# Performance work log

Measured on AMD Instinct MI355X. Metric: run time of the kernel, lower is better.

Reference implementation:

```python
import jax, jax.numpy as jnp
import numpy as np

D = 8  # polynomial degree; with bias present, basis has D columns (P1..PD)


def setup_inputs() -> dict:
    key = jax.random.key(0)
    k1, k2 = jax.random.split(key)
    batch, n_in, n_out = 65536, 256, 64
    x = jax.random.normal(k1, (batch, n_in), dtype=jnp.float32)
    c_basis = jax.random.normal(k2, (n_out, n_in, D), dtype=jnp.float32) * (1.0 / np.sqrt(n_in * D))
    bias = jnp.zeros((n_out,), dtype=jnp.float32)
    return {"x": x, "c_basis": c_basis, "bias": bias}


def _legendre_basis(x):
    # x: (batch, n_in). Returns (batch, n_in, D) = [P1(t), ..., PD(t)], t = tanh(x).
    t = jnp.tanh(x)
    p_prev = jnp.ones_like(t)  # P0
    p_curr = t                 # P1
    polys = [p_curr]
    for k in range(2, D + 1):  # small fixed-length loop over degree
        p_next = ((2 * k - 1) * t * p_curr - (k - 1) * p_prev) / k
        polys.append(p_next)
        p_prev, p_curr = p_curr, p_next
    return jnp.stack(polys, axis=-1)  # (batch, n_in, D)


def reference(x, c_basis, bias):
    # basis: (batch, n_in, D); contract over (n_in, D) with c_basis (n_out, n_in, D)
    leg = _legendre_basis(x)
    y = jnp.einsum('bid,oid->bo', leg, c_basis)
    return y + bias
```

## Files before the change

kernel.cpp:

```cpp
#include <hip/hip_runtime.h>
#include <hip/hip_bf16.h>

typedef _Float16 half2v __attribute__((ext_vector_type(2)));
typedef _Float16 half8  __attribute__((ext_vector_type(8)));
typedef __attribute__((ext_vector_type(4))) float floatx4;
typedef __attribute__((ext_vector_type(4))) unsigned int uintx4;

#define GLOBAL_AS __attribute__((address_space(1)))
#define LDS_AS __attribute__((address_space(3)))

__device__ __forceinline__ void async_ld16(const void* g, void* l) {
  __builtin_amdgcn_global_load_lds((const GLOBAL_AS unsigned int*)g,
                                   (LDS_AS unsigned int*)l, 16, 0, 0);
}

__device__ __forceinline__ half2v h2(float v) {
  return (half2v){(_Float16)v, (_Float16)v};
}

__device__ __forceinline__ void legendre2_f16(float xv0, float xv1,
                                              half8* fa0, half8* fa1) {
  float e0 = __builtin_amdgcn_exp2f(xv0 * 2.885390081777927f);
  float t0 = 1.0f - 2.0f * __builtin_amdgcn_rcpf(e0 + 1.0f);
  float e1 = __builtin_amdgcn_exp2f(xv1 * 2.885390081777927f);
  float t1 = 1.0f - 2.0f * __builtin_amdgcn_rcpf(e1 + 1.0f);
  half2v t;
  { auto tt = __builtin_amdgcn_cvt_pkrtz(t0, t1); __builtin_memcpy(&t, &tt, 4); }
  half2v p1 = t;
  half2v u2 = t * p1, w2 = u2 - h2(1.0f);  half2v p2 = h2(0.5f)      * w2 + u2;
  half2v u3 = t * p2, w3 = u3 - p1;        half2v p3 = h2(2.0f/3.0f) * w3 + u3;
  half2v u4 = t * p3, w4 = u4 - p2;        half2v p4 = h2(0.75f)     * w4 + u4;
  half2v u5 = t * p4, w5 = u5 - p3;        half2v p5 = h2(0.8f)      * w5 + u5;
  half2v u6 = t * p5, w6 = u6 - p4;        half2v p6 = h2(5.0f/6.0f) * w6 + u6;
  half2v u7 = t * p6, w7 = u7 - p5;        half2v p7 = h2(6.0f/7.0f) * w7 + u7;
  half2v u8 = t * p7, w8 = u8 - p6;        half2v p8 = h2(7.0f/8.0f) * w8 + u8;
  unsigned P[8];
  __builtin_memcpy(&P[0], &p1, 4); __builtin_memcpy(&P[1], &p2, 4);
  __builtin_memcpy(&P[2], &p3, 4); __builtin_memcpy(&P[3], &p4, 4);
  __builtin_memcpy(&P[4], &p5, 4); __builtin_memcpy(&P[5], &p6, 4);
  __builtin_memcpy(&P[6], &p7, 4); __builtin_memcpy(&P[7], &p8, 4);
  union { unsigned u[4]; half8 h; } a0, a1;
#pragma unroll
  for (int j = 0; j < 4; ++j) {
    a0.u[j] = __builtin_amdgcn_perm(P[2*j+1], P[2*j], 0x05040100u);
    a1.u[j] = __builtin_amdgcn_perm(P[2*j+1], P[2*j], 0x07060302u);
  }
  *fa0 = a0.h;
  *fa1 = a1.h;
}

__global__ void conv_kernel(const float* __restrict__ cb, _Float16* __restrict__ ws) {
  int t = blockIdx.x * 128 + threadIdx.x;
  int o = t >> 8;
  int i = t & 255;
  const floatx4* s = (const floatx4*)(cb + ((size_t)o * 256 + i) * 8);
  floatx4 v0 = s[0], v1 = s[1];
  union { _Float16 h[8]; uintx4 u; } w;
  w.h[0] = (_Float16)v0.x; w.h[1] = (_Float16)v0.y;
  w.h[2] = (_Float16)v0.z; w.h[3] = (_Float16)v0.w;
  w.h[4] = (_Float16)v1.x; w.h[5] = (_Float16)v1.y;
  w.h[6] = (_Float16)v1.z; w.h[7] = (_Float16)v1.w;
  *(uintx4*)(ws + (size_t)i * 512 + o * 8) = w.u;
}

#define MB 64
#define NCH 16

__global__ __launch_bounds__(128, 2) void kan_kernel(
    const float* __restrict__ x, const _Float16* __restrict__ ws,
    const float* __restrict__ bias, float* __restrict__ y) {
  __shared__ __align__(16) _Float16 bt[2][16 * 64 * 8];
  __shared__ __align__(16) float xs[2][MB * 16];

  const int tid  = threadIdx.x;
  const int wid  = tid >> 6;
  const int lane = tid & 63;
  const int m    = lane & 15;
  const int q    = lane >> 4;
  const int row_block = blockIdx.x * MB;

  floatx4 acc[2][4];
#pragma unroll
  for (int a = 0; a < 2; ++a)
#pragma unroll
    for (int nt = 0; nt < 4; ++nt) acc[a][nt] = (floatx4){0.f, 0.f, 0.f, 0.f};

  const _Float16* bsrc[8];
#pragma unroll
  for (int t = 0; t < 8; ++t)
    bsrc[t] = ws + (size_t)(t * 128 + wid * 64 + lane) * 8;
  const float* xsrc[2];
#pragma unroll
  for (int t = 0; t < 2; ++t) {
    int slot = t * 128 + wid * 64 + lane;
    int r = slot >> 2;
    int c4 = (slot & 3) ^ (r & 3);
    xsrc[t] = x + (size_t)(row_block + r) * 256 + c4 * 4;
  }

  auto stage = [&](int buf) {
#pragma unroll
    for (int t = 0; t < 8; ++t) {
      int sb = t * 128 + wid * 64;
      async_ld16(bsrc[t], &bt[buf][sb * 8]);
      bsrc[t] += 8192;
    }
#pragma unroll
    for (int t = 0; t < 2; ++t) {
      int sb = t * 128 + wid * 64;
      async_ld16(xsrc[t], &xs[buf][sb * 4]);
      xsrc[t] += 16;
    }
  };

  const int xoff0 = (wid * 32 + m) * 64 + ((m & 3) << 4) + q * 4;
  const int xoff1 = xoff0 + 1024;

  stage(0);
#pragma unroll 2
  for (int ch = 0; ch < NCH; ++ch) {
    const int buf = ch & 1;
    asm volatile("s_barrier" ::: "memory");
    if (ch + 1 < NCH) {
      stage(buf ^ 1);
      asm volatile("s_waitcnt vmcnt(10)" ::: "memory");
    } else {
      asm volatile("s_waitcnt vmcnt(0)" ::: "memory");
    }
    asm volatile("s_barrier" ::: "memory");

    const _Float16* bp = &bt[buf][q * 512 + m * 8];
    const char* xb = (const char*)&xs[buf][0];
#pragma unroll
    for (int ks = 0; ks < 4; ++ks) {
      half8 fb0 = *(const half8*)(bp + ks * 2048 + 0 * 128);
      half8 fb1 = *(const half8*)(bp + ks * 2048 + 1 * 128);
      half8 fb2 = *(const half8*)(bp + ks * 2048 + 2 * 128);
      half8 fb3 = *(const half8*)(bp + ks * 2048 + 3 * 128);
      float xv0 = *(const float*)(xb + (xoff0 ^ (ks << 4)));
      float xv1 = *(const float*)(xb + (xoff1 ^ (ks << 4)));
      half8 fa0, fa1;
      legendre2_f16(xv0, xv1, &fa0, &fa1);
      acc[0][0] = __builtin_amdgcn_mfma_f32_16x16x32_f16(fa0, fb0, acc[0][0], 0, 0, 0);
      acc[1][0] = __builtin_amdgcn_mfma_f32_16x16x32_f16(fa1, fb0, acc[1][0], 0, 0, 0);
      acc[0][1] = __builtin_amdgcn_mfma_f32_16x16x32_f16(fa0, fb1, acc[0][1], 0, 0, 0);
      acc[1][1] = __builtin_amdgcn_mfma_f32_16x16x32_f16(fa1, fb1, acc[1][1], 0, 0, 0);
      acc[0][2] = __builtin_amdgcn_mfma_f32_16x16x32_f16(fa0, fb2, acc[0][2], 0, 0, 0);
      acc[1][2] = __builtin_amdgcn_mfma_f32_16x16x32_f16(fa1, fb2, acc[1][2], 0, 0, 0);
      acc[0][3] = __builtin_amdgcn_mfma_f32_16x16x32_f16(fa0, fb3, acc[0][3], 0, 0, 0);
      acc[1][3] = __builtin_amdgcn_mfma_f32_16x16x32_f16(fa1, fb3, acc[1][3], 0, 0, 0);
    }
  }

  float bv[4];
#pragma unroll
  for (int nt = 0; nt < 4; ++nt) bv[nt] = bias[nt * 16 + m];
#pragma unroll
  for (int a = 0; a < 2; ++a) {
    int gr0 = row_block + wid * 32 + a * 16 + q * 4;
#pragma unroll
    for (int nt = 0; nt < 4; ++nt) {
#pragma unroll
      for (int r = 0; r < 4; ++r) {
        y[(size_t)(gr0 + r) * 64 + nt * 16 + m] = acc[a][nt][r] + bv[nt];
      }
    }
  }
}

extern "C" void kernel_launch(void* const* d_in, const int* in_sizes, int n_in,
                              void* d_out, int out_size, void* d_ws, size_t ws_size,
                              hipStream_t stream) {
  const float* x    = (const float*)d_in[0];
  const float* cb   = (const float*)d_in[1];
  const float* bias = (const float*)d_in[2];
  float* y = (float*)d_out;
  _Float16* ws = (_Float16*)d_ws;
  int batch = in_sizes[0] / 256;
  hipLaunchKernelGGL(conv_kernel, dim3(128), dim3(128), 0, stream, cb, ws);
  hipLaunchKernelGGL(kan_kernel, dim3(batch / MB), dim3(128), 0, stream, x, ws, bias, y);
}
```

Measured before the change: 120.4 us.

## Load x directly into registers with prefetch and compute Legendre before barrier

Stops staging x through LDS. Each lane now loads four contiguous float columns straight into registers, prefetched two chunks ahead. The Legendre basis for the whole chunk is computed before the barrier and wait, so the transcendental math overlaps the async weight loads, and the B-fragment indexing is remapped to match the new k ordering. MFMA issue is wrapped in s_setprio to favour the matrix phase, at the cost of more live registers for the prefetch and precomputed fragments.

```diff
diff --git a/kernel.cpp b/kernel.cpp
--- a/kernel.cpp
+++ b/kernel.cpp
@@ -2,7 +2,7 @@
 #include <hip/hip_bf16.h>
 
 typedef _Float16 half2v __attribute__((ext_vector_type(2)));
-typedef _Float16 half8  __attribute__((ext_vector_type(8)));
+typedef _Float16 half8 __attribute__((ext_vector_type(8)));
 typedef __attribute__((ext_vector_type(4))) float floatx4;
 typedef __attribute__((ext_vector_type(4))) unsigned int uintx4;
 
@@ -63,21 +63,19 @@
   *(uintx4*)(ws + (size_t)i * 512 + o * 8) = w.u;
 }
 
-#define MB 64
 #define NCH 16
 
 __global__ __launch_bounds__(128, 2) void kan_kernel(
     const float* __restrict__ x, const _Float16* __restrict__ ws,
     const float* __restrict__ bias, float* __restrict__ y) {
   __shared__ __align__(16) _Float16 bt[2][16 * 64 * 8];
-  __shared__ __align__(16) float xs[2][MB * 16];
 
   const int tid  = threadIdx.x;
   const int wid  = tid >> 6;
   const int lane = tid & 63;
   const int m    = lane & 15;
   const int q    = lane >> 4;
-  const int row_block = blockIdx.x * MB;
+  const int row_block = blockIdx.x * 64;
 
   floatx4 acc[2][4];
 #pragma unroll
@@ -89,67 +87,72 @@
 #pragma unroll
   for (int t = 0; t < 8; ++t)
     bsrc[t] = ws + (size_t)(t * 128 + wid * 64 + lane) * 8;
-  const float* xsrc[2];
-#pragma unroll
-  for (int t = 0; t < 2; ++t) {
-    int slot = t * 128 + wid * 64 + lane;
-    int r = slot >> 2;
-    int c4 = (slot & 3) ^ (r & 3);
-    xsrc[t] = x + (size_t)(row_block + r) * 256 + c4 * 4;
-  }
 
-  auto stage = [&](int buf) {
+  const float* xp0 = x + (size_t)(row_block + wid * 32 + m) * 256 + q * 4;
+  const float* xp1 = xp0 + 16 * 256;
+
+  floatx4 xa0 = *(const floatx4*)xp0;
+  floatx4 xa1 = *(const floatx4*)xp1;
+  floatx4 xb0 = *(const floatx4*)(xp0 + 16);
+  floatx4 xb1 = *(const floatx4*)(xp1 + 16);
+  xp0 += 32; xp1 += 32;
+
+  auto stage = [&](int b) {
 #pragma unroll
     for (int t = 0; t < 8; ++t) {
       int sb = t * 128 + wid * 64;
-      async_ld16(bsrc[t], &bt[buf][sb * 8]);
+      async_ld16(bsrc[t], &bt[b][sb * 8]);
       bsrc[t] += 8192;
-    }
-#pragma unroll
-    for (int t = 0; t < 2; ++t) {
-      int sb = t * 128 + wid * 64;
-      async_ld16(xsrc[t], &xs[buf][sb * 4]);
-      xsrc[t] += 16;
     }
   };
 
-  const int xoff0 = (wid * 32 + m) * 64 + ((m & 3) << 4) + q * 4;
-  const int xoff1 = xoff0 + 1024;
+  stage(0);
 
-  stage(0);
 #pragma unroll 2
   for (int ch = 0; ch < NCH; ++ch) {
     const int buf = ch & 1;
+
+    half8 f0[4], f1[4];
+#pragma unroll
+    for (int j = 0; j < 4; ++j)
+      legendre2_f16(xa0[j], xa1[j], &f0[j], &f1[j]);
+
     asm volatile("s_barrier" ::: "memory");
+
+    floatx4 xn0 = xb0, xn1 = xb1;
     if (ch + 1 < NCH) {
       stage(buf ^ 1);
+      if (ch + 2 < NCH) {
+        xn0 = *(const floatx4*)xp0;
+        xn1 = *(const floatx4*)xp1;
+        xp0 += 16; xp1 += 16;
+      }
       asm volatile("s_waitcnt vmcnt(10)" ::: "memory");
     } else {
       asm volatile("s_waitcnt vmcnt(0)" ::: "memory");
     }
     asm volatile("s_barrier" ::: "memory");
 
-    const _Float16* bp = &bt[buf][q * 512 + m * 8];
-    const char* xb = (const char*)&xs[buf][0];
+    __builtin_amdgcn_s_setprio(1);
+    const _Float16* bp = &bt[buf][q * 2048 + m * 8];
 #pragma unroll
-    for (int ks = 0; ks < 4; ++ks) {
-      half8 fb0 = *(const half8*)(bp + ks * 2048 + 0 * 128);
-      half8 fb1 = *(const half8*)(bp + ks * 2048 + 1 * 128);
-      half8 fb2 = *(const half8*)(bp + ks * 2048 + 2 * 128);
-      half8 fb3 = *(const half8*)(bp + ks * 2048 + 3 * 128);
-      float xv0 = *(const float*)(xb + (xoff0 ^ (ks << 4)));
-      float xv1 = *(const float*)(xb + (xoff1 ^ (ks << 4)));
-      half8 fa0, fa1;
-      legendre2_f16(xv0, xv1, &fa0, &fa1);
-      acc[0][0] = __builtin_amdgcn_mfma_f32_16x16x32_f16(fa0, fb0, acc[0][0], 0, 0, 0);
-      acc[1][0] = __builtin_amdgcn_mfma_f32_16x16x32_f16(fa1, fb0, acc[1][0], 0, 0, 0);
-      acc[0][1] = __builtin_amdgcn_mfma_f32_16x16x32_f16(fa0, fb1, acc[0][1], 0, 0, 0);
-      acc[1][1] = __builtin_amdgcn_mfma_f32_16x16x32_f16(fa1, fb1, acc[1][1], 0, 0, 0);
-      acc[0][2] = __builtin_amdgcn_mfma_f32_16x16x32_f16(fa0, fb2, acc[0][2], 0, 0, 0);
-      acc[1][2] = __builtin_amdgcn_mfma_f32_16x16x32_f16(fa1, fb2, acc[1][2], 0, 0, 0);
-      acc[0][3] = __builtin_amdgcn_mfma_f32_16x16x32_f16(fa0, fb3, acc[0][3], 0, 0, 0);
-      acc[1][3] = __builtin_amdgcn_mfma_f32_16x16x32_f16(fa1, fb3, acc[1][3], 0, 0, 0);
+    for (int j = 0; j < 4; ++j) {
+      half8 fb0 = *(const half8*)(bp + j * 512 + 0 * 128);
+      half8 fb1 = *(const half8*)(bp + j * 512 + 1 * 128);
+      half8 fb2 = *(const half8*)(bp + j * 512 + 2 * 128);
+      half8 fb3 = *(const half8*)(bp + j * 512 + 3 * 128);
+      acc[0][0] = __builtin_amdgcn_mfma_f32_16x16x32_f16(f0[j], fb0, acc[0][0], 0, 0, 0);
+      acc[1][0] = __builtin_amdgcn_mfma_f32_16x16x32_f16(f1[j], fb0, acc[1][0], 0, 0, 0);
+      acc[0][1] = __builtin_amdgcn_mfma_f32_16x16x32_f16(f0[j], fb1, acc[0][1], 0, 0, 0);
+      acc[1][1] = __builtin_amdgcn_mfma_f32_16x16x32_f16(f1[j], fb1, acc[1][1], 0, 0, 0);
+      acc[0][2] = __builtin_amdgcn_mfma_f32_16x16x32_f16(f0[j], fb2, acc[0][2], 0, 0, 0);
+      acc[1][2] = __builtin_amdgcn_mfma_f32_16x16x32_f16(f1[j], fb2, acc[1][2], 0, 0, 0);
+      acc[0][3] = __builtin_amdgcn_mfma_f32_16x16x32_f16(f0[j], fb3, acc[0][3], 0, 0, 0);
+      acc[1][3] = __builtin_amdgcn_mfma_f32_16x16x32_f16(f1[j], fb3, acc[1][3], 0, 0, 0);
     }
+    __builtin_amdgcn_s_setprio(0);
+
+    xa0 = xb0; xa1 = xb1; xb0 = xn0; xb1 = xn1;
   }
 
   float bv[4];
@@ -178,5 +181,5 @@
   _Float16* ws = (_Float16*)d_ws;
   int batch = in_sizes[0] / 256;
   hipLaunchKernelGGL(conv_kernel, dim3(128), dim3(128), 0, stream, cb, ws);
-  hipLaunchKernelGGL(kan_kernel, dim3(batch / MB), dim3(128), 0, stream, x, ws, bias, y);
+  hipLaunchKernelGGL(kan_kernel, dim3(batch / 64), dim3(128), 0, stream, x, ws, bias, y);
 }
```

Result: no change. 121.4 us (+0.8%).
